# Kernel tuning notes

Measured on AMD Instinct MI355X. Metric: run time of the kernel, lower is better.

Reference implementation:

```python
import jax, jax.numpy as jnp
import numpy as np

B, T, D, H = 4, 2048, 1024, 16
DH = D // H  # 64


def setup_inputs() -> dict:
    key = jax.random.key(0)
    k1, k2, k3 = jax.random.split(key, 3)
    x = jax.random.normal(k1, (B, T, D), dtype=jnp.float32)
    w_qkv = jax.random.normal(k2, (D, 3 * D), dtype=jnp.float32) * (D ** -0.5)
    w_out = jax.random.normal(k3, (D, D), dtype=jnp.float32) * (D ** -0.5)
    return {"x": x, "w_qkv": w_qkv, "w_out": w_out}


def reference(x, w_qkv, w_out):
    b, t, d = x.shape
    qkv = jnp.einsum('btd,de->bte', x, w_qkv)  # [B,T,3D]
    q, k, v = jnp.split(qkv, 3, axis=-1)
    # [B,H,T,DH]
    q = q.reshape(b, t, H, DH).transpose(0, 2, 1, 3)
    k = k.reshape(b, t, H, DH).transpose(0, 2, 1, 3)
    v = v.reshape(b, t, H, DH).transpose(0, 2, 1, 3)
    logits = jnp.einsum('bhqd,bhkd->bhqk', q, k) * (1.0 / jnp.sqrt(jnp.float32(DH)))
    # causal bias: -inf strictly above the diagonal (key index > query index)
    causal = jnp.tril(jnp.ones((t, t), dtype=bool))
    logits = jnp.where(causal, logits, jnp.float32(-jnp.inf))
    scores = jax.nn.softmax(logits, axis=-1)
    y = jnp.einsum('bhqk,bhkd->bhqd', scores, v)
    y = y.transpose(0, 2, 1, 3).reshape(b, t, d)
    return jnp.einsum('btd,de->bte', y, w_out)
```

## Files before the change

kernel.cpp:

```cpp
#include <hip/hip_runtime.h>
#include <hip/hip_bf16.h>


namespace {
constexpr int kB = 4, kT = 2048, kD = 1024, kH = 16;
constexpr int kM = kB * kT;
constexpr int kNq = 3 * kD;
constexpr float kS = 0.180336880f;
}

typedef unsigned short u16;
typedef short bf16x8 __attribute__((ext_vector_type(8)));
typedef float f32x4 __attribute__((ext_vector_type(4)));

__device__ __forceinline__ u16 f2bf(float f) {
  unsigned int u = __float_as_uint(f);
  u += 0x7fffu + ((u >> 16) & 1u);
  return (u16)(u >> 16);
}
__device__ __forceinline__ unsigned int pack2(float a, float b) {
  return (unsigned int)f2bf(a) | ((unsigned int)f2bf(b) << 16);
}
__device__ __forceinline__ unsigned int cvtpk(float a, float b) {
  unsigned int r;
  asm("v_cvt_pk_bf16_f32 %0, %1, %2" : "=v"(r) : "v"(a), "v"(b));
  return r;
}

__device__ __forceinline__ void gload16(const u16* g, u16* l) {
  __builtin_amdgcn_global_load_lds(
      (const __attribute__((address_space(1))) unsigned int*)(uintptr_t)g,
      (__attribute__((address_space(3))) unsigned int*)(uintptr_t)l, 16, 0, 0);
}

__global__ __launch_bounds__(256) void prep(const float* __restrict__ x,
                                            u16* __restrict__ xb,
                                            const float* __restrict__ wq,
                                            u16* __restrict__ wqT,
                                            const float* __restrict__ wo,
                                            u16* __restrict__ woT) {
  __shared__ float T[32][33];
  const int tid = threadIdx.x;
  const int id = blockIdx.x;
  if (id < 4096) {
    const size_t i = ((size_t)id * 256 + tid) * 8;
    const float4 v0 = *(const float4*)(x + i);
    const float4 v1 = *(const float4*)(x + i + 4);
    uint4 p;
    p.x = pack2(v0.x, v0.y);
    p.y = pack2(v0.z, v0.w);
    p.z = pack2(v1.x, v1.y);
    p.w = pack2(v1.z, v1.w);
    *(uint4*)(xb + i) = p;
    return;
  }
  const float* W;
  u16* WT;
  int N, nscale, nb, kb;
  if (id < 4096 + 3072) {
    const int t = id - 4096;
    W = wq; WT = wqT; N = kNq; nscale = kD;
    nb = (t % 96) * 32; kb = (t / 96) * 32;
  } else {
    const int t = id - 7168;
    W = wo; WT = woT; N = kD; nscale = 0;
    nb = (t & 31) * 32; kb = (t >> 5) * 32;
  }
  const int r = tid >> 3, c = (tid & 7) * 4;
  const float4 v = *(const float4*)&W[(size_t)(kb + r) * N + nb + c];
  T[r][c + 0] = v.x;
  T[r][c + 1] = v.y;
  T[r][c + 2] = v.z;
  T[r][c + 3] = v.w;
  __syncthreads();
  const float s = (nb + r < nscale) ? kS : 1.0f;
  uint2 p;
  p.x = pack2(T[c + 0][r] * s, T[c + 1][r] * s);
  p.y = pack2(T[c + 2][r] * s, T[c + 3][r] * s);
  *(uint2*)&WT[(size_t)(nb + r) * kD + kb + c] = p;
}

template <bool F32OUT>
__global__ __launch_bounds__(512, 2) void gemm256b(const u16* __restrict__ A,
                                                   const u16* __restrict__ BT,
                                                   void* __restrict__ Cv,
                                                   int lda, int ldc) {
  __shared__ u16 As[2][256 * 64];
  __shared__ u16 Bs[2][256 * 64];
  constexpr int NT = kD / 64;
  const int tid = threadIdx.x;
  const int wid = tid >> 6, lane = tid & 63;
  const int col = lane & 15, quad = lane >> 4;
  const int wm_ = wid >> 2, wn_ = wid & 3;

  const int nwg = gridDim.x * gridDim.y;
  int flat = blockIdx.y * gridDim.x + blockIdx.x;
  flat = (flat & 7) * (nwg >> 3) + (flat >> 3);
  const int n0 = (flat % gridDim.x) * 256;
  const int m0 = (flat / gridDim.x) * 256;

  const int srow = tid >> 3;
  const int scol8 = (tid & 7) * 8;
  const int gch8 = ((tid & 7) ^ (srow & 7)) * 8;
  const u16* const Ag = A + (size_t)(m0 + srow) * lda + gch8;
  const u16* const Bg = BT + (size_t)(n0 + srow) * kD + gch8;

  f32x4 acc[8][4];
#pragma unroll
  for (int i = 0; i < 8; ++i)
#pragma unroll
    for (int j = 0; j < 4; ++j) acc[i][j] = (f32x4){0.f, 0.f, 0.f, 0.f};

#define STAGE_AH(buf, half, k0)                                      \
  do {                                                               \
    gload16(Ag + (size_t)((half)*128) * lda + (k0),                  \
            &As[buf][((half)*128 + srow) * 64 + scol8]);             \
    gload16(Ag + (size_t)((half)*128 + 64) * lda + (k0),             \
            &As[buf][((half)*128 + 64 + srow) * 64 + scol8]);        \
  } while (0)
#define STAGE_BH(buf, half, k0)                                      \
  do {                                                               \
    gload16(Bg + (size_t)((half)*128) * kD + (k0),                   \
            &Bs[buf][((half)*128 + srow) * 64 + scol8]);             \
    gload16(Bg + (size_t)((half)*128 + 64) * kD + (k0),              \
            &Bs[buf][((half)*128 + 64 + srow) * 64 + scol8]);        \
  } while (0)

  STAGE_AH(0, 0, 0);
  STAGE_BH(0, 0, 0);
  STAGE_BH(0, 1, 0);
  STAGE_AH(0, 1, 0);
  STAGE_AH(1, 0, 64);
  STAGE_BH(1, 0, 64);
  asm volatile("s_waitcnt vmcnt(4)" ::: "memory");
  __builtin_amdgcn_s_barrier();

  for (int t = 0; t < NT; ++t) {
    const int cur = t & 1, nxt = cur ^ 1;
    const u16* Ac = &As[cur][0];
    const u16* Bc = &Bs[cur][0];
    const int k1 = (t + 1) * 64;
    const int k2 = (t + 2) * 64;
    const bool pf1 = (t + 1 < NT);
    const bool pf2 = (t + 2 < NT);
    bf16x8 af[4], bv[4];

#define READ_A(KS, MH)                                                        \
  do {                                                                        \
    _Pragma("unroll") for (int mi = 0; mi < 4; ++mi) {                        \
      const int r = (MH)*128 + wm_ * 64 + mi * 16 + col;                      \
      af[mi] =                                                                \
          *(const bf16x8*)&Ac[r * 64 + ((((KS)*4 + quad) ^ (r & 7)) * 8)];    \
    }                                                                         \
  } while (0)
#define READ_B(KS)                                                            \
  do {                                                                        \
    _Pragma("unroll") for (int ni = 0; ni < 4; ++ni) {                        \
      const int r = wn_ * 64 + ni * 16 + col;                                 \
      bv[ni] =                                                                \
          *(const bf16x8*)&Bc[r * 64 + ((((KS)*4 + quad) ^ (r & 7)) * 8)];    \
    }                                                                         \
  } while (0)
#define MFMA16(MH)                                                            \
  do {                                                                        \
    __builtin_amdgcn_s_setprio(1);                                            \
    _Pragma("unroll") for (int mi = 0; mi < 4; ++mi)                          \
        _Pragma("unroll") for (int ni = 0; ni < 4; ++ni) acc[(MH)*4 + mi][ni] \
        = __builtin_amdgcn_mfma_f32_16x16x32_bf16(af[mi], bv[ni],             \
                                                  acc[(MH)*4 + mi][ni], 0, 0, \
                                                  0);                         \
    __builtin_amdgcn_s_setprio(0);                                            \
  } while (0)

    READ_A(0, 0);
    READ_B(0);
    if (pf1) STAGE_BH(nxt, 1, k1);
    __builtin_amdgcn_s_barrier();
    asm volatile("s_waitcnt lgkmcnt(0)" ::: "memory");
    MFMA16(0);
    if (pf1)
      asm volatile("s_waitcnt vmcnt(6)" ::: "memory");
    else
      asm volatile("s_waitcnt vmcnt(0)" ::: "memory");
    __builtin_amdgcn_s_barrier();

    READ_A(0, 1);
    if (pf1) STAGE_AH(nxt, 1, k1);
    __builtin_amdgcn_s_barrier();
    asm volatile("s_waitcnt lgkmcnt(0)" ::: "memory");
    MFMA16(1);
    __builtin_amdgcn_s_barrier();

    READ_A(1, 0);
    READ_B(1);
    __builtin_amdgcn_s_barrier();
    asm volatile("s_waitcnt lgkmcnt(0)" ::: "memory");
    MFMA16(0);
    __builtin_amdgcn_s_barrier();

    READ_A(1, 1);
    if (pf2) {
      STAGE_AH(cur, 0, k2);
      STAGE_BH(cur, 0, k2);
    }
    __builtin_amdgcn_s_barrier();
    asm volatile("s_waitcnt lgkmcnt(0)" ::: "memory");
    MFMA16(1);
    if (pf2)
      asm volatile("s_waitcnt vmcnt(6)" ::: "memory");
    else if (pf1)
      asm volatile("s_waitcnt vmcnt(2)" ::: "memory");
    __builtin_amdgcn_s_barrier();

#undef READ_A
#undef READ_B
#undef MFMA16
  }
#undef STAGE_AH
#undef STAGE_BH

#pragma unroll
  for (int mig = 0; mig < 8; ++mig) {
    const int row =
        m0 + (mig >> 2) * 128 + wm_ * 64 + (mig & 3) * 16 + quad * 4;
#pragma unroll
    for (int reg = 0; reg < 4; ++reg) {
#pragma unroll
      for (int nig = 0; nig < 4; ++nig) {
        const int cc = n0 + wn_ * 64 + nig * 16 + col;
        if (F32OUT)
          ((float*)Cv)[(size_t)(row + reg) * ldc + cc] = acc[mig][nig][reg];
        else
          ((u16*)Cv)[(size_t)(row + reg) * ldc + cc] = f2bf(acc[mig][nig][reg]);
      }
    }
  }
}

template <bool F32OUT>
__global__ __launch_bounds__(512, 2) void gemm_mt(const u16* __restrict__ A,
                                                  const u16* __restrict__ BT,
                                                  void* __restrict__ Cv,
                                                  int lda, int ldc) {
  __shared__ u16 As[2][256 * 64];
  __shared__ u16 Bs[2][128 * 64];
  constexpr int NT = kD / 64;
  const int tid = threadIdx.x;
  const int wid = tid >> 6, lane = tid & 63;
  const int col = lane & 15, quad = lane >> 4;
  const int wm_ = wid >> 2, wn_ = wid & 3;

  const int nwg = gridDim.x * gridDim.y;
  int flat = blockIdx.y * gridDim.x + blockIdx.x;
  flat = (flat & 7) * (nwg >> 3) + (flat >> 3);
  const int n0 = (flat % gridDim.x) * 128;
  const int m0 = (flat / gridDim.x) * 256;

  const int srow = tid >> 3;
  const int scol8 = (tid & 7) * 8;
  const int gch8 = ((tid & 7) ^ (srow & 7)) * 8;
  const u16* const Ag = A + (size_t)(m0 + srow) * lda + gch8;
  const u16* const Bg = BT + (size_t)(n0 + srow) * kD + gch8;

  f32x4 acc[8][2];
#pragma unroll
  for (int i = 0; i < 8; ++i)
#pragma unroll
    for (int j = 0; j < 2; ++j) acc[i][j] = (f32x4){0.f, 0.f, 0.f, 0.f};

#define STAGE_AH(buf, half, k0)                                      \
  do {                                                               \
    gload16(Ag + (size_t)((half)*128) * lda + (k0),                  \
            &As[buf][((half)*128 + srow) * 64 + scol8]);             \
    gload16(Ag + (size_t)((half)*128 + 64) * lda + (k0),             \
            &As[buf][((half)*128 + 64 + srow) * 64 + scol8]);        \
  } while (0)
#define STAGE_BF(buf, k0)                                            \
  do {                                                               \
    gload16(Bg + (size_t)(k0), &Bs[buf][srow * 64 + scol8]);         \
    gload16(Bg + (size_t)64 * kD + (k0),                             \
            &Bs[buf][(64 + srow) * 64 + scol8]);                     \
  } while (0)

  STAGE_AH(0, 0, 0);
  STAGE_BF(0, 0);
  STAGE_AH(0, 1, 0);
  STAGE_AH(1, 0, 64);
  STAGE_BF(1, 64);
  asm volatile("s_waitcnt vmcnt(4)" ::: "memory");
  __builtin_amdgcn_s_barrier();

  for (int t = 0; t < NT; ++t) {
    const int cur = t & 1;
    const u16* Ac = &As[cur][0];
    const u16* Bc = &Bs[cur][0];
    bf16x8 af[4][2], bv[2][2];

#pragma unroll
    for (int mi = 0; mi < 4; ++mi) {
      const int r = wm_ * 64 + mi * 16 + col;
#pragma unroll
      for (int ks = 0; ks < 2; ++ks)
        af[mi][ks] =
            *(const bf16x8*)&Ac[r * 64 + (((ks * 4 + quad) ^ (r & 7)) * 8)];
    }
#pragma unroll
    for (int ni = 0; ni < 2; ++ni) {
      const int r = wn_ * 32 + ni * 16 + col;
#pragma unroll
      for (int ks = 0; ks < 2; ++ks)
        bv[ni][ks] =
            *(const bf16x8*)&Bc[r * 64 + (((ks * 4 + quad) ^ (r & 7)) * 8)];
    }
    if (t + 1 < NT) STAGE_AH(cur ^ 1, 1, (t + 1) * 64);
    __builtin_amdgcn_s_barrier();
    asm volatile("s_waitcnt lgkmcnt(0)" ::: "memory");
    __builtin_amdgcn_s_setprio(1);
#pragma unroll
    for (int mi = 0; mi < 4; ++mi)
#pragma unroll
      for (int ni = 0; ni < 2; ++ni)
#pragma unroll
        for (int ks = 0; ks < 2; ++ks)
          acc[mi][ni] = __builtin_amdgcn_mfma_f32_16x16x32_bf16(
              af[mi][ks], bv[ni][ks], acc[mi][ni], 0, 0, 0);
    __builtin_amdgcn_s_setprio(0);
    if (t + 1 < NT)
      asm volatile("s_waitcnt vmcnt(6)" ::: "memory");
    else
      asm volatile("s_waitcnt vmcnt(0)" ::: "memory");
    __builtin_amdgcn_s_barrier();

#pragma unroll
    for (int mi = 0; mi < 4; ++mi) {
      const int r = 128 + wm_ * 64 + mi * 16 + col;
#pragma unroll
      for (int ks = 0; ks < 2; ++ks)
        af[mi][ks] =
            *(const bf16x8*)&Ac[r * 64 + (((ks * 4 + quad) ^ (r & 7)) * 8)];
    }
    if (t + 2 < NT) {
      STAGE_AH(cur, 0, (t + 2) * 64);
      STAGE_BF(cur, (t + 2) * 64);
    }
    __builtin_amdgcn_s_barrier();
    asm volatile("s_waitcnt lgkmcnt(0)" ::: "memory");
    __builtin_amdgcn_s_setprio(1);
#pragma unroll
    for (int mi = 0; mi < 4; ++mi)
#pragma unroll
      for (int ni = 0; ni < 2; ++ni)
#pragma unroll
        for (int ks = 0; ks < 2; ++ks)
          acc[4 + mi][ni] = __builtin_amdgcn_mfma_f32_16x16x32_bf16(
              af[mi][ks], bv[ni][ks], acc[4 + mi][ni], 0, 0, 0);
    __builtin_amdgcn_s_setprio(0);
    if (t + 2 < NT)
      asm volatile("s_waitcnt vmcnt(6)" ::: "memory");
    else if (t + 1 < NT)
      asm volatile("s_waitcnt vmcnt(2)" ::: "memory");
    __builtin_amdgcn_s_barrier();
  }
#undef STAGE_AH
#undef STAGE_BF

#pragma unroll
  for (int mh = 0; mh < 2; ++mh)
#pragma unroll
    for (int mi = 0; mi < 4; ++mi) {
      const int row = m0 + mh * 128 + wm_ * 64 + mi * 16 + quad * 4;
#pragma unroll
      for (int reg = 0; reg < 4; ++reg) {
#pragma unroll
        for (int ni = 0; ni < 2; ++ni) {
          const int cc = n0 + wn_ * 32 + ni * 16 + col;
          if (F32OUT)
            ((float*)Cv)[(size_t)(row + reg) * ldc + cc] =
                acc[mh * 4 + mi][ni][reg];
          else
            ((u16*)Cv)[(size_t)(row + reg) * ldc + cc] =
                f2bf(acc[mh * 4 + mi][ni][reg]);
        }
      }
    }
}

__global__ __launch_bounds__(256) void attn_fwd(u16* __restrict__ qkv) {
  __shared__ u16 Ks[2][64 * 64];
  __shared__ u16 Vt[64][68];
  __shared__ u16 Ps[64][68];
  const int tid = threadIdx.x;
  const int w = tid >> 6, lane = tid & 63;
  const int col = lane & 15, quad = lane >> 4;
  const int bh = blockIdx.x;
  const int b = bh >> 4, h = bh & 15;
  const int pa = blockIdx.y;
  const size_t base = (size_t)(b * kT) * kNq + h * 64;

  const int krr = lane >> 3;
  const int ksw = (lane & 7) ^ krr;
  const u16* const kgbase =
      qkv + base + kD + (size_t)(w * 16 + krr) * kNq + ksw * 8;

  const int vkp = (tid & 31) * 2, vd0 = (tid >> 5) * 8;
  const u16* const vgbase = qkv + base + 2 * kD + (size_t)vkp * kNq + vd0;

  bf16x8 onesf;
#pragma unroll
  for (int i = 0; i < 8; ++i) onesf[i] = (short)0x3F80;

  int cur = 0;
#pragma unroll
  for (int pass = 0; pass < 2; ++pass) {
    const int qt = pass ? (31 - pa) : pa;
    const int q0 = qt << 6;

    bf16x8 aq[2];
#pragma unroll
    for (int ks = 0; ks < 2; ++ks)
      aq[ks] = *(const bf16x8*)(qkv + base + (size_t)(q0 + w * 16 + col) * kNq +
                                ks * 32 + quad * 8);

    gload16(kgbase, &Ks[cur][(w * 16) * 64]);
    gload16(kgbase + (size_t)8 * kNq, &Ks[cur][(w * 16 + 8) * 64]);
    uint4 va = *(const uint4*)vgbase;
    uint4 vb = *(const uint4*)(vgbase + kNq);

    f32x4 o[4];
#pragma unroll
    for (int nt = 0; nt < 4; ++nt) o[nt] = (f32x4){0.f, 0.f, 0.f, 0.f};
    f32x4 o4 = (f32x4){0.f, 0.f, 0.f, 0.f};

    for (int kt = 0; kt <= qt; ++kt) {
      __syncthreads();
      {
        const unsigned int* aw = (const unsigned int*)&va;
        const unsigned int* bw = (const unsigned int*)&vb;
#pragma unroll
        for (int i = 0; i < 4; ++i) {
          *(unsigned int*)&Vt[vd0 + 2 * i][vkp] =
              __builtin_amdgcn_perm(bw[i], aw[i], 0x05040100u);
          *(unsigned int*)&Vt[vd0 + 2 * i + 1][vkp] =
              __builtin_amdgcn_perm(bw[i], aw[i], 0x07060302u);
        }
      }
      __syncthreads();

      if (kt < qt) {
        const size_t ko = (size_t)((kt + 1) << 6) * kNq;
        gload16(kgbase + ko, &Ks[cur ^ 1][(w * 16) * 64]);
        gload16(kgbase + ko + (size_t)8 * kNq, &Ks[cur ^ 1][(w * 16 + 8) * 64]);
        va = *(const uint4*)(vgbase + ko);
        vb = *(const uint4*)(vgbase + ko + kNq);
      }

      f32x4 st[4];
#pragma unroll
      for (int nt = 0; nt < 4; ++nt) st[nt] = (f32x4){0.f, 0.f, 0.f, 0.f};
#pragma unroll
      for (int ks = 0; ks < 2; ++ks) {
#pragma unroll
        for (int nt = 0; nt < 4; ++nt) {
          const int kr = nt * 16 + col;
          const bf16x8 bk =
              *(const bf16x8*)&Ks[cur][kr * 64 +
                                       (((ks * 4 + quad) ^ (col & 7)) * 8)];
          st[nt] = __builtin_amdgcn_mfma_f32_16x16x32_bf16(bk, aq[ks], st[nt],
                                                           0, 0, 0);
        }
      }

      if (kt == qt) {
        const int qrel = w * 16 + col;
#pragma unroll
        for (int nt = 0; nt < 4; ++nt)
#pragma unroll
          for (int reg = 0; reg < 4; ++reg) {
            const int krel = nt * 16 + quad * 4 + reg;
            st[nt][reg] =
                (krel <= qrel) ? __builtin_amdgcn_exp2f(st[nt][reg]) : 0.f;
          }
      } else {
#pragma unroll
        for (int nt = 0; nt < 4; ++nt)
#pragma unroll
          for (int reg = 0; reg < 4; ++reg)
            st[nt][reg] = __builtin_amdgcn_exp2f(st[nt][reg]);
      }

#pragma unroll
      for (int nt = 0; nt < 4; ++nt) {
        uint2 pk;
        pk.x = cvtpk(st[nt][0], st[nt][1]);
        pk.y = cvtpk(st[nt][2], st[nt][3]);
        *(uint2*)&Ps[w * 16 + col][nt * 16 + quad * 4] = pk;
      }

#pragma unroll
      for (int ks = 0; ks < 2; ++ks) {
        const bf16x8 ap =
            *(const bf16x8*)&Ps[w * 16 + col][ks * 32 + quad * 8];
#pragma unroll
        for (int nt = 0; nt < 4; ++nt) {
          const bf16x8 bv =
              *(const bf16x8*)&Vt[nt * 16 + col][ks * 32 + quad * 8];
          o[nt] = __builtin_amdgcn_mfma_f32_16x16x32_bf16(ap, bv, o[nt], 0, 0,
                                                          0);
        }
        o4 = __builtin_amdgcn_mfma_f32_16x16x32_bf16(ap, onesf, o4, 0, 0, 0);
      }
      cur ^= 1;
    }

#pragma unroll
    for (int reg = 0; reg < 4; ++reg) {
      const float inv = 1.0f / o4[reg];
      u16* yp = qkv + base + (size_t)(q0 + w * 16 + quad * 4 + reg) * kNq;
#pragma unroll
      for (int nt = 0; nt < 4; ++nt)
        yp[nt * 16 + col] = f2bf(o[nt][reg] * inv);
    }
  }
}

extern "C" void kernel_launch(void* const* d_in, const int* in_sizes, int n_in,
                              void* d_out, int out_size, void* d_ws,
                              size_t ws_size, hipStream_t stream) {
  const float* x = (const float*)d_in[0];
  const float* w_qkv = (const float*)d_in[1];
  const float* w_out = (const float*)d_in[2];

  u16* wqkvT = (u16*)d_ws;
  u16* woutT = wqkvT + (size_t)kNq * kD;
  u16* qkvb = woutT + (size_t)kD * kD;
  u16* xb = (u16*)d_out;

  prep<<<8192, 256, 0, stream>>>(x, xb, w_qkv, wqkvT, w_out, woutT);
  gemm256b<false><<<dim3(kNq / 256, kM / 256), 512, 0, stream>>>(xb, wqkvT,
                                                                 qkvb, kD,
                                                                 kNq);
  attn_fwd<<<dim3(kB * kH, 16), 256, 0, stream>>>(qkvb);
  gemm_mt<true><<<dim3(kD / 128, kM / 256), 512, 0, stream>>>(qkvb, woutT,
                                                              d_out, kNq, kD);
}
```

Baseline: 237.4 us.

## Double-buffer transposed V tile and XOR-swizzle Vt/Ps shared layouts in attention

Makes the transposed V tile double-buffered in shared memory. The next tile's V is written during the current iteration, so the loop needs one barrier per iteration instead of two. The padded Vt and Ps arrays become 64-wide rows with XOR swizzling on 8-element chunks, to avoid LDS bank conflicts on the MFMA operand reads. V global loads are issued two tiles ahead, which adds register pressure and uses more shared memory per block.

```diff
diff --git a/kernel.cpp b/kernel.cpp
--- a/kernel.cpp
+++ b/kernel.cpp
@@ -387,8 +387,8 @@
 
 __global__ __launch_bounds__(256) void attn_fwd(u16* __restrict__ qkv) {
   __shared__ u16 Ks[2][64 * 64];
-  __shared__ u16 Vt[64][68];
-  __shared__ u16 Ps[64][68];
+  __shared__ u16 Vt[2][64 * 64];
+  __shared__ u16 Ps[64 * 64];
   const int tid = threadIdx.x;
   const int w = tid >> 6, lane = tid & 63;
   const int col = lane & 15, quad = lane >> 4;
@@ -404,12 +404,25 @@
 
   const int vkp = (tid & 31) * 2, vd0 = (tid >> 5) * 8;
   const u16* const vgbase = qkv + base + 2 * kD + (size_t)vkp * kNq + vd0;
+  const int vch = vkp >> 3, vin = vkp & 7;
 
   bf16x8 onesf;
 #pragma unroll
   for (int i = 0; i < 8; ++i) onesf[i] = (short)0x3F80;
 
-  int cur = 0;
+#define WRITE_VT(buf)                                                         \
+  do {                                                                        \
+    const unsigned int* aw_ = (const unsigned int*)&va;                       \
+    const unsigned int* bw_ = (const unsigned int*)&vb;                       \
+    _Pragma("unroll") for (int i = 0; i < 4; ++i) {                           \
+      const int r0_ = vd0 + 2 * i, r1_ = r0_ + 1;                             \
+      *(unsigned int*)&Vt[buf][r0_ * 64 + ((vch ^ (r0_ & 7)) * 8) + vin] =    \
+          __builtin_amdgcn_perm(bw_[i], aw_[i], 0x05040100u);                 \
+      *(unsigned int*)&Vt[buf][r1_ * 64 + ((vch ^ (r1_ & 7)) * 8) + vin] =    \
+          __builtin_amdgcn_perm(bw_[i], aw_[i], 0x07060302u);                 \
+    }                                                                         \
+  } while (0)
+
 #pragma unroll
   for (int pass = 0; pass < 2; ++pass) {
     const int qt = pass ? (31 - pa) : pa;
@@ -421,8 +434,8 @@
       aq[ks] = *(const bf16x8*)(qkv + base + (size_t)(q0 + w * 16 + col) * kNq +
                                 ks * 32 + quad * 8);
 
-    gload16(kgbase, &Ks[cur][(w * 16) * 64]);
-    gload16(kgbase + (size_t)8 * kNq, &Ks[cur][(w * 16 + 8) * 64]);
+    gload16(kgbase, &Ks[0][(w * 16) * 64]);
+    gload16(kgbase + (size_t)8 * kNq, &Ks[0][(w * 16 + 8) * 64]);
     uint4 va = *(const uint4*)vgbase;
     uint4 vb = *(const uint4*)(vgbase + kNq);
 
@@ -431,27 +444,21 @@
     for (int nt = 0; nt < 4; ++nt) o[nt] = (f32x4){0.f, 0.f, 0.f, 0.f};
     f32x4 o4 = (f32x4){0.f, 0.f, 0.f, 0.f};
 
+    __syncthreads();
+    WRITE_VT(0);
+    if (qt > 0) {
+      va = *(const uint4*)(vgbase + (size_t)64 * kNq);
+      vb = *(const uint4*)(vgbase + (size_t)65 * kNq);
+    }
+    __syncthreads();
+
+    int cur = 0;
     for (int kt = 0; kt <= qt; ++kt) {
-      __syncthreads();
-      {
-        const unsigned int* aw = (const unsigned int*)&va;
-        const unsigned int* bw = (const unsigned int*)&vb;
-#pragma unroll
-        for (int i = 0; i < 4; ++i) {
-          *(unsigned int*)&Vt[vd0 + 2 * i][vkp] =
-              __builtin_amdgcn_perm(bw[i], aw[i], 0x05040100u);
-          *(unsigned int*)&Vt[vd0 + 2 * i + 1][vkp] =
-              __builtin_amdgcn_perm(bw[i], aw[i], 0x07060302u);
-        }
-      }
-      __syncthreads();
-
+      const int nxt = cur ^ 1;
       if (kt < qt) {
         const size_t ko = (size_t)((kt + 1) << 6) * kNq;
-        gload16(kgbase + ko, &Ks[cur ^ 1][(w * 16) * 64]);
-        gload16(kgbase + ko + (size_t)8 * kNq, &Ks[cur ^ 1][(w * 16 + 8) * 64]);
-        va = *(const uint4*)(vgbase + ko);
-        vb = *(const uint4*)(vgbase + ko + kNq);
+        gload16(kgbase + ko, &Ks[nxt][(w * 16) * 64]);
+        gload16(kgbase + ko + (size_t)8 * kNq, &Ks[nxt][(w * 16 + 8) * 64]);
       }
 
       f32x4 st[4];
@@ -493,23 +500,38 @@
         uint2 pk;
         pk.x = cvtpk(st[nt][0], st[nt][1]);
         pk.y = cvtpk(st[nt][2], st[nt][3]);
-        *(uint2*)&Ps[w * 16 + col][nt * 16 + quad * 4] = pk;
+        *(uint2*)&Ps[(w * 16 + col) * 64 +
+                     (((nt * 2 + (quad >> 1)) ^ (col & 7)) * 8) +
+                     (quad & 1) * 4] = pk;
+      }
+
+      if (kt < qt) {
+        WRITE_VT(nxt);
+        if (kt + 1 < qt) {
+          const size_t ko2 = (size_t)((kt + 2) << 6) * kNq;
+          va = *(const uint4*)(vgbase + ko2);
+          vb = *(const uint4*)(vgbase + ko2 + kNq);
+        }
       }
 
 #pragma unroll
       for (int ks = 0; ks < 2; ++ks) {
         const bf16x8 ap =
-            *(const bf16x8*)&Ps[w * 16 + col][ks * 32 + quad * 8];
+            *(const bf16x8*)&Ps[(w * 16 + col) * 64 +
+                                (((ks * 4 + quad) ^ (col & 7)) * 8)];
 #pragma unroll
         for (int nt = 0; nt < 4; ++nt) {
           const bf16x8 bv =
-              *(const bf16x8*)&Vt[nt * 16 + col][ks * 32 + quad * 8];
+              *(const bf16x8*)&Vt[cur][(nt * 16 + col) * 64 +
+                                       (((ks * 4 + quad) ^ (col & 7)) * 8)];
           o[nt] = __builtin_amdgcn_mfma_f32_16x16x32_bf16(ap, bv, o[nt], 0, 0,
                                                           0);
         }
         o4 = __builtin_amdgcn_mfma_f32_16x16x32_bf16(ap, onesf, o4, 0, 0, 0);
       }
-      cur ^= 1;
+
+      __syncthreads();
+      cur = nxt;
     }
 
 #pragma unroll
@@ -521,6 +543,7 @@
         yp[nt * 16 + col] = f2bf(o[nt][reg] * inv);
     }
   }
+#undef WRITE_VT
 }
 
 extern "C" void kernel_launch(void* const* d_in, const int* in_sizes, int n_in,
```

New measurement: 259.9 us. 1.09x slower.
